# Kernel tuning notes

Hardware: AMD Instinct MI355X
Metric: run time of the kernel (lower is better)

The kernel has to match this reference:

```python
import jax, jax.numpy as jnp
from jax import lax
import numpy as np

B, T = 256, 100
N_FEAT, V, E, H = 64, 32, 8, 512
CAT_POS = np.arange(0, N_FEAT, 4)                                 # 16 categorical feature indices
CONT_POS = np.array([k for k in range(N_FEAT) if k % 4 != 0])      # 48 continuous feature indices
N_CAT, N_CONT = len(CAT_POS), len(CONT_POS)
IN_LEN = N_FEAT + N_CAT * (E - 1)                                  # 176, matches input_linear.in_features
N_LAYERS = 2                                                        # len(hidden_layers) - 1 LSTMs

# Precompute the interleaved output layout of embed(): walking feature index k,
# categorical features occupy E slots, continuous features 1 slot.
def _layout():
    cont_off, cat_off, cur = [], [], 0
    for k in range(N_FEAT):
        if k % 4 == 0:
            cat_off.append(cur); cur += E
        else:
            cont_off.append(cur); cur += 1
    return np.array(cont_off), np.array(cat_off)
CONT_OFF, CAT_OFF = _layout()
CAT_COLS = (CAT_OFF[:, None] + np.arange(E)).ravel()               # [N_CAT*E] target columns


def lstm(x, Wih, Whh, bih, bhh):
    # PyTorch LSTM, batch_first, gate order (i, f, g, o).
    xw = jnp.einsum('bti,gi->btg', x, Wih) + bih                   # [B,T,4H] input projection (one GEMM)
    def step(carry, xw_t):
        h, c = carry
        gates = xw_t + h @ Whh.T + bhh
        i, f, g, o = jnp.split(gates, 4, axis=-1)
        c = jax.nn.sigmoid(f) * c + jax.nn.sigmoid(i) * jnp.tanh(g)
        h = jax.nn.sigmoid(o) * jnp.tanh(c)
        return (h, c), h
    h0 = jnp.zeros((x.shape[0], Whh.shape[1]), x.dtype)
    (_, _), hs = lax.scan(step, (h0, h0), jnp.swapaxes(xw, 0, 1))
    return jnp.swapaxes(hs, 0, 1)                                   # [B,T,H]


def setup_inputs() -> dict:
    key = jax.random.key(0)
    ks = jax.random.split(key, 16)
    s = 0.05
    base = jax.random.normal(ks[0], (B, T, N_FEAT), jnp.float32)
    cats = jax.random.randint(ks[1], (B, T, N_CAT), 0, V)
    x = base.at[..., CAT_POS].set(cats.astype(jnp.float32))
    return {
        'x': x,
        'scaler_mean': jax.random.normal(ks[2], (N_FEAT,), jnp.float32),
        'scaler_scale': jax.random.uniform(ks[3], (N_FEAT,), jnp.float32, minval=0.5, maxval=2.0),
        'emb': jax.random.normal(ks[4], (N_CAT, V, E), jnp.float32) * s,
        'W_in': jax.random.normal(ks[5], (IN_LEN, H), jnp.float32) * s,
        'b_in': jnp.zeros((H,), jnp.float32),
        'Wih': jax.random.normal(ks[6], (N_LAYERS, 4 * H, H), jnp.float32) * s,
        'Whh': jax.random.normal(ks[7], (N_LAYERS, 4 * H, H), jnp.float32) * s,
        'bih': jnp.zeros((N_LAYERS, 4 * H), jnp.float32),
        'bhh': jnp.zeros((N_LAYERS, 4 * H), jnp.float32),
        'W_out': jax.random.normal(ks[8], (H, N_CONT), jnp.float32) * s,
        'b_out': jnp.zeros((N_CONT,), jnp.float32),
        'W_cls': jax.random.normal(ks[9], (N_CAT, H, V), jnp.float32) * s,
        'b_cls': jnp.zeros((N_CAT, V), jnp.float32),
    }


def reference(x, scaler_mean, scaler_scale, emb, W_in, b_in, Wih, Whh, bih, bhh, W_out, b_out, W_cls, b_cls):
    # ---- embed(): vectorized replacement of the triple python loop ----
    scaled = (x - scaler_mean) / scaler_scale                      # sklearn StandardScaler.transform
    cont_vals = scaled[..., CONT_POS]                              # [B,T,48]
    idx = x[..., CAT_POS].astype(jnp.int32)                        # [B,T,16] categorical codes
    embv = emb[jnp.arange(N_CAT)[None, None, :], idx]              # [B,T,16,E] gather
    new = jnp.zeros((x.shape[0], x.shape[1], IN_LEN), x.dtype)
    new = new.at[..., CONT_OFF].set(cont_vals)
    new = new.at[..., CAT_COLS].set(embv.reshape(x.shape[0], x.shape[1], N_CAT * E))
    # ---- input linear + activation ----
    h = jax.nn.relu(new @ W_in + b_in)                             # [B,T,512]
    # ---- stacked LSTMs, activation after each ----
    for l in range(N_LAYERS):
        h = jax.nn.relu(lstm(h, Wih[l], Whh[l], bih[l], bhh[l]))
    last = h[:, -1, :]                                             # [B,512]
    cont_out = last @ W_out + b_out                                # [B,48]
    cls_out = jnp.einsum('bh,nhv->bnv', last, W_cls) + b_cls       # [B,16,32] classification heads
    return (cont_out, cls_out)
```

## Files before the change

### kernel.cpp

```cpp
#include <hip/hip_runtime.h>

#define BB 256
#define TT 100
#define HH 512
#define G4 2048
#define INL 176
#define KIN 192
#define NCAT 16
#define NCONT 48
#define VV 32
#define EE 8
#define MTOT (BB*TT)
#define GRPB 32

typedef unsigned short u16;
typedef unsigned int   u32;
typedef unsigned long long u64;
typedef __attribute__((ext_vector_type(8))) short bf16x8;
typedef __attribute__((ext_vector_type(4))) float f32x4;

__device__ __forceinline__ float bf2f(u16 u){
    union { u32 i; float f; } v; v.i = ((u32)u) << 16; return v.f;
}
__device__ __forceinline__ u16 f2bf(float f){
    union { float f; u32 i; } v; v.f = f;
    u32 b = v.i;
    b += 0x7FFFu + ((b >> 16) & 1u);
    return (u16)(b >> 16);
}
__device__ __forceinline__ float fast_tanh(float x){
    float e = __expf(2.f * x);
    return 1.f - 2.f / (e + 1.f);
}

__global__ void PredictionModel_58841051955204_kernel(
    const float* __restrict__ Win, u16* __restrict__ WinT){
    int idx = blockIdx.x*256 + threadIdx.x;
    if (idx >= HH*KIN) return;
    int h = idx / KIN, i = idx % KIN;
    WinT[idx] = (i < INL) ? f2bf(Win[i*HH + h]) : (u16)0;
}

__global__ void k_cvt(const float* __restrict__ in, u16* __restrict__ out, int n){
    int i = blockIdx.x*256 + threadIdx.x;
    if (i < n) out[i] = f2bf(in[i]);
}

__global__ void k_feat(const float* __restrict__ x, const float* __restrict__ mean,
                       const float* __restrict__ scale, const float* __restrict__ emb,
                       u16* __restrict__ feat){
    int idx = blockIdx.x*256 + threadIdx.x;
    int bt = idx >> 4, g = idx & 15;
    if (bt >= MTOT) return;
    const float* xr = x + (size_t)bt*64;
    u16* fr = feat + (size_t)bt*KIN;
    int k0 = g*4;
    int ci = (int)xr[k0];
    if (ci < 0) ci = 0;
    if (ci > VV-1) ci = VV-1;
    const float* ep = emb + (size_t)(g*VV + ci)*EE;
    int c0 = g*11;
    for (int e = 0; e < 8; e++) fr[c0+e] = f2bf(ep[e]);
    for (int j = 1; j <= 3; j++){
        int k = k0 + j;
        fr[c0 + 8 + (j-1)] = f2bf((xr[k] - mean[k]) / scale[k]);
    }
    fr[INL + g] = 0;
}

__global__ __launch_bounds__(256) void k_gemm(
    const u16* __restrict__ A, int lda,
    const u16* __restrict__ W, int K,
    const float* __restrict__ bias1, const float* __restrict__ bias2,
    void* __restrict__ out, int ldo, int kc_cnt, int do_relu, int out_half)
{
    __shared__ u16 sA[64*40];
    __shared__ u16 sB[256*40];
    int tid = threadIdx.x;
    int w = tid >> 6, lane = tid & 63, q = lane >> 4, r = lane & 15;
    int m0 = blockIdx.x * 64;
    int n0 = blockIdx.y * 256;

    f32x4 acc[4][4];
    for (int a_ = 0; a_ < 4; a_++)
        for (int b_ = 0; b_ < 4; b_++){
            acc[a_][b_][0] = 0.f; acc[a_][b_][1] = 0.f;
            acc[a_][b_][2] = 0.f; acc[a_][b_][3] = 0.f;
        }

    for (int kc = 0; kc < kc_cnt; kc++){
        {
            int row = tid >> 2, seg = tid & 3;
            uint4 v = *(const uint4*)(A + (size_t)(m0+row)*lda + kc*32 + seg*8);
            *(uint4*)(&sA[row*40 + seg*8]) = v;
            const u16* wr = W + (size_t)(n0 + tid)*K + kc*32;
            uint4 b0 = *(const uint4*)(wr);
            uint4 b1 = *(const uint4*)(wr+8);
            uint4 b2 = *(const uint4*)(wr+16);
            uint4 b3 = *(const uint4*)(wr+24);
            u16* d = &sB[tid*40];
            *(uint4*)(d)    = b0; *(uint4*)(d+8)  = b1;
            *(uint4*)(d+16) = b2; *(uint4*)(d+24) = b3;
        }
        __syncthreads();
        bf16x8 a[4], b[4];
        for (int mt = 0; mt < 4; mt++) a[mt] = *(const bf16x8*)(&sA[(mt*16 + r)*40 + q*8]);
        for (int i = 0; i < 4; i++)    b[i]  = *(const bf16x8*)(&sB[((w*4+i)*16 + r)*40 + q*8]);
        for (int mt = 0; mt < 4; mt++)
            for (int i = 0; i < 4; i++)
                acc[mt][i] = __builtin_amdgcn_mfma_f32_16x16x32_bf16(a[mt], b[i], acc[mt][i], 0, 0, 0);
        __syncthreads();
    }

    for (int i = 0; i < 4; i++){
        int n = n0 + (w*4+i)*16 + r;
        float bs = 0.f;
        if (bias1) bs += bias1[n];
        if (bias2) bs += bias2[n];
        for (int mt = 0; mt < 4; mt++){
            for (int reg = 0; reg < 4; reg++){
                int m = m0 + mt*16 + q*4 + reg;
                float v = acc[mt][i][reg] + bs;
                if (do_relu) v = fmaxf(v, 0.f);
                if (out_half) ((_Float16*)out)[(size_t)m*ldo + n] = (_Float16)v;
                else          ((u16*)out)[(size_t)m*ldo + n] = f2bf(v);
            }
        }
    }
}

__global__ void k_zcnt(int* bar){
    int i = blockIdx.x*256 + threadIdx.x;
    if (i < 2*4*GRPB*16) bar[i] = 0;
}

__global__ __launch_bounds__(256, 1) void k_rec2(
    const u16* __restrict__ Whhb,
    const u16* __restrict__ Wihb1,
    const _Float16* __restrict__ xw,
    const float* __restrict__ bih, const float* __restrict__ bhh,
    u64* __restrict__ h0A, u64* __restrict__ h0B,
    u64* __restrict__ x0r,
    u64* __restrict__ h1A, u64* __restrict__ h1B,
    int* __restrict__ bar)
{
    extern __shared__ u16 smem[];
    int tid = threadIdx.x;
    int w = tid >> 6, lane = tid & 63, q = lane >> 4, r = lane & 15;
    int lay  = blockIdx.x >> 7;
    int bid7 = blockIdx.x & 127;
    int mg = bid7 & 3, jb = bid7 >> 2;
    int m0 = mg*64, j0 = jb*16;
    int j = j0 + r;
    int* F0 = bar + mg*(GRPB*16);
    int* F1 = bar + 4*(GRPB*16) + mg*(GRPB*16);

    {
        int row = tid >> 2, seg = tid & 3;
        int g = row >> 4, jj = row & 15;
        const u16* srcW = Whhb + (size_t)lay*G4*HH + (size_t)(g*HH + j0 + jj)*HH;
        u16* sW = smem + (lay ? 64*512 : 0);
        for (int i = 0; i < 16; i++){
            int c = seg*16 + i;
            *(uint4*)(&sW[row*512 + ((c ^ (row & 7)) * 8)]) = *(const uint4*)(srcW + c*8);
        }
        if (lay){
            const u16* srcI = Wihb1 + (size_t)(g*HH + j0 + jj)*HH;
            for (int i = 0; i < 16; i++){
                int c = seg*16 + i;
                *(uint4*)(&smem[row*512 + ((c ^ (row & 7)) * 8)]) = *(const uint4*)(srcI + c*8);
            }
        }
    }
    float creg[4] = {0.f, 0.f, 0.f, 0.f};
    {
        u64* hz = lay ? h1A : h0A;
        if ((r & 3) == 0){
            for (int reg = 0; reg < 4; reg++){
                int m = m0 + w*16 + q*4 + reg;
                __hip_atomic_store(&hz[(size_t)m*(HH/4) + ((j0 + r) >> 2)], 0ULL,
                                   __ATOMIC_RELAXED, __HIP_MEMORY_SCOPE_AGENT);
            }
        }
    }
    float bs1[4] = {0.f, 0.f, 0.f, 0.f};
    if (lay){
        for (int g = 0; g < 4; g++)
            bs1[g] = bih[G4 + g*HH + j] + bhh[G4 + g*HH + j];
    }
    float xnxt[4][4];
    if (!lay){
        #pragma unroll
        for (int reg = 0; reg < 4; reg++){
            int m = m0 + w*16 + q*4 + reg;
            const _Float16* xr = xw + ((size_t)m*TT + 0)*G4 + j;
            #pragma unroll
            for (int g = 0; g < 4; g++)
                xnxt[reg][g] = (float)__builtin_nontemporal_load(xr + g*HH);
        }
    }

    for (int t = -1; t < TT; t++){
        if (t >= 0 && !lay){
            const u64* hsrc = (t & 1) ? h0B : h0A;
            u64*       hdst = (t & 1) ? h0A : h0B;
            u32* xdst32 = (u32*)(x0r + (size_t)(t & 3)*BB*(HH/4));
            const u64* hrow = hsrc + (size_t)(m0 + w*16 + r)*(HH/4);

            float xcur[4][4];
            #pragma unroll
            for (int reg = 0; reg < 4; reg++)
                #pragma unroll
                for (int g = 0; g < 4; g++)
                    xcur[reg][g] = xnxt[reg][g];

            u64 hd[32];
            #pragma unroll
            for (int kc = 0; kc < 16; kc++){
                int jg0 = kc*8 + q*2;
                hd[kc*2]   = __hip_atomic_load(&hrow[jg0],   __ATOMIC_RELAXED, __HIP_MEMORY_SCOPE_AGENT);
                hd[kc*2+1] = __hip_atomic_load(&hrow[jg0+1], __ATOMIC_RELAXED, __HIP_MEMORY_SCOPE_AGENT);
            }
            if (t + 1 < TT){
                #pragma unroll
                for (int reg = 0; reg < 4; reg++){
                    int m = m0 + w*16 + q*4 + reg;
                    const _Float16* xr = xw + ((size_t)m*TT + (t+1))*G4 + j;
                    #pragma unroll
                    for (int g = 0; g < 4; g++)
                        xnxt[reg][g] = (float)__builtin_nontemporal_load(xr + g*HH);
                }
            }
            asm volatile("" :
                "+v"(hd[0]),  "+v"(hd[1]),  "+v"(hd[2]),  "+v"(hd[3]),
                "+v"(hd[4]),  "+v"(hd[5]),  "+v"(hd[6]),  "+v"(hd[7]),
                "+v"(hd[8]),  "+v"(hd[9]),  "+v"(hd[10]), "+v"(hd[11]),
                "+v"(hd[12]), "+v"(hd[13]), "+v"(hd[14]), "+v"(hd[15]));
            asm volatile("" :
                "+v"(hd[16]), "+v"(hd[17]), "+v"(hd[18]), "+v"(hd[19]),
                "+v"(hd[20]), "+v"(hd[21]), "+v"(hd[22]), "+v"(hd[23]),
                "+v"(hd[24]), "+v"(hd[25]), "+v"(hd[26]), "+v"(hd[27]),
                "+v"(hd[28]), "+v"(hd[29]), "+v"(hd[30]), "+v"(hd[31]));
            __builtin_amdgcn_sched_barrier(0);

            f32x4 acc[4];
            for (int g = 0; g < 4; g++){
                acc[g][0] = 0.f; acc[g][1] = 0.f; acc[g][2] = 0.f; acc[g][3] = 0.f;
            }
            #pragma unroll
            for (int kc = 0; kc < 16; kc++){
                union { u64 d[2]; bf16x8 v; } au;
                au.d[0] = hd[kc*2];
                au.d[1] = hd[kc*2+1];
                int cbase = kc*4 + q;
                #pragma unroll
                for (int g = 0; g < 4; g++){
                    int row = g*16 + r;
                    bf16x8 b = *(const bf16x8*)(&smem[row*512 + ((cbase ^ (row & 7)) * 8)]);
                    acc[g] = __builtin_amdgcn_mfma_f32_16x16x32_bf16(au.v, b, acc[g], 0, 0, 0);
                }
            }

            u32* hdst32 = (u32*)hdst;
            #pragma unroll
            for (int reg = 0; reg < 4; reg++){
                int m = m0 + w*16 + q*4 + reg;
                float Gi = acc[0][reg] + xcur[reg][0];
                float Gf = acc[1][reg] + xcur[reg][1];
                float Gg = acc[2][reg] + xcur[reg][2];
                float Go = acc[3][reg] + xcur[reg][3];
                float iv = 1.f/(1.f + __expf(-Gi));
                float fv = 1.f/(1.f + __expf(-Gf));
                float gv = fast_tanh(Gg);
                float ov = 1.f/(1.f + __expf(-Go));
                float c = fv * creg[reg] + iv * gv;
                creg[reg] = c;
                float h = ov * fast_tanh(c);
                u32 own  = (u32)f2bf(h);
                u32 ownr = (u32)f2bf(fmaxf(h, 0.f));
                u32 p01  = own  | (((u32)__shfl_xor((int)own,  1)) << 16);
                u32 pr01 = ownr | (((u32)__shfl_xor((int)ownr, 1)) << 16);
                if ((r & 1) == 0){
                    size_t ofs = (size_t)m*(HH/2) + ((j0 + r) >> 1);
                    __hip_atomic_store(&hdst32[ofs], p01, __ATOMIC_RELAXED, __HIP_MEMORY_SCOPE_AGENT);
                    __hip_atomic_store(&xdst32[ofs], pr01, __ATOMIC_RELAXED, __HIP_MEMORY_SCOPE_AGENT);
                }
            }
        } else if (t >= 0 && lay){
            const u64* xsrc = x0r + (size_t)(t & 3)*BB*(HH/4);
            const u64* hsrc = (t & 1) ? h1B : h1A;
            u64*       hdst = (t & 1) ? h1A : h1B;
            const u64* xrow = xsrc + (size_t)(m0 + w*16 + r)*(HH/4);
            const u64* hrow = hsrc + (size_t)(m0 + w*16 + r)*(HH/4);
            const u16* sWih = smem;
            const u16* sWhh = smem + 64*512;

            u64 hx[32], hh[32];
            #pragma unroll
            for (int kc = 0; kc < 16; kc++){
                int jg0 = kc*8 + q*2;
                hx[kc*2]   = __hip_atomic_load(&xrow[jg0],   __ATOMIC_RELAXED, __HIP_MEMORY_SCOPE_AGENT);
                hx[kc*2+1] = __hip_atomic_load(&xrow[jg0+1], __ATOMIC_RELAXED, __HIP_MEMORY_SCOPE_AGENT);
            }
            #pragma unroll
            for (int kc = 0; kc < 16; kc++){
                int jg0 = kc*8 + q*2;
                hh[kc*2]   = __hip_atomic_load(&hrow[jg0],   __ATOMIC_RELAXED, __HIP_MEMORY_SCOPE_AGENT);
                hh[kc*2+1] = __hip_atomic_load(&hrow[jg0+1], __ATOMIC_RELAXED, __HIP_MEMORY_SCOPE_AGENT);
            }
            asm volatile("" :
                "+v"(hx[0]),  "+v"(hx[1]),  "+v"(hx[2]),  "+v"(hx[3]),
                "+v"(hx[4]),  "+v"(hx[5]),  "+v"(hx[6]),  "+v"(hx[7]),
                "+v"(hx[8]),  "+v"(hx[9]),  "+v"(hx[10]), "+v"(hx[11]),
                "+v"(hx[12]), "+v"(hx[13]), "+v"(hx[14]), "+v"(hx[15]));
            asm volatile("" :
                "+v"(hx[16]), "+v"(hx[17]), "+v"(hx[18]), "+v"(hx[19]),
                "+v"(hx[20]), "+v"(hx[21]), "+v"(hx[22]), "+v"(hx[23]),
                "+v"(hx[24]), "+v"(hx[25]), "+v"(hx[26]), "+v"(hx[27]),
                "+v"(hx[28]), "+v"(hx[29]), "+v"(hx[30]), "+v"(hx[31]));
            __builtin_amdgcn_sched_barrier(0);

            f32x4 acc[4];
            for (int g = 0; g < 4; g++){
                acc[g][0] = 0.f; acc[g][1] = 0.f; acc[g][2] = 0.f; acc[g][3] = 0.f;
            }
            #pragma unroll
            for (int kc = 0; kc < 16; kc++){
                union { u64 d[2]; bf16x8 v; } au;
                au.d[0] = hx[kc*2];
                au.d[1] = hx[kc*2+1];
                int cbase = kc*4 + q;
                #pragma unroll
                for (int g = 0; g < 4; g++){
                    int row = g*16 + r;
                    bf16x8 b = *(const bf16x8*)(&sWih[row*512 + ((cbase ^ (row & 7)) * 8)]);
                    acc[g] = __builtin_amdgcn_mfma_f32_16x16x32_bf16(au.v, b, acc[g], 0, 0, 0);
                }
            }
            asm volatile("" :
                "+v"(hh[0]),  "+v"(hh[1]),  "+v"(hh[2]),  "+v"(hh[3]),
                "+v"(hh[4]),  "+v"(hh[5]),  "+v"(hh[6]),  "+v"(hh[7]),
                "+v"(hh[8]),  "+v"(hh[9]),  "+v"(hh[10]), "+v"(hh[11]),
                "+v"(hh[12]), "+v"(hh[13]), "+v"(hh[14]), "+v"(hh[15]));
            asm volatile("" :
                "+v"(hh[16]), "+v"(hh[17]), "+v"(hh[18]), "+v"(hh[19]),
                "+v"(hh[20]), "+v"(hh[21]), "+v"(hh[22]), "+v"(hh[23]),
                "+v"(hh[24]), "+v"(hh[25]), "+v"(hh[26]), "+v"(hh[27]),
                "+v"(hh[28]), "+v"(hh[29]), "+v"(hh[30]), "+v"(hh[31]));
            #pragma unroll
            for (int kc = 0; kc < 16; kc++){
                union { u64 d[2]; bf16x8 v; } au;
                au.d[0] = hh[kc*2];
                au.d[1] = hh[kc*2+1];
                int cbase = kc*4 + q;
                #pragma unroll
                for (int g = 0; g < 4; g++){
                    int row = g*16 + r;
                    bf16x8 b = *(const bf16x8*)(&sWhh[row*512 + ((cbase ^ (row & 7)) * 8)]);
                    acc[g] = __builtin_amdgcn_mfma_f32_16x16x32_bf16(au.v, b, acc[g], 0, 0, 0);
                }
            }

            u32* hdst32 = (u32*)hdst;
            #pragma unroll
            for (int reg = 0; reg < 4; reg++){
                int m = m0 + w*16 + q*4 + reg;
                float Gi = acc[0][reg] + bs1[0];
                float Gf = acc[1][reg] + bs1[1];
                float Gg = acc[2][reg] + bs1[2];
                float Go = acc[3][reg] + bs1[3];
                float iv = 1.f/(1.f + __expf(-Gi));
                float fv = 1.f/(1.f + __expf(-Gf));
                float gv = fast_tanh(Gg);
                float ov = 1.f/(1.f + __expf(-Go));
                float c = fv * creg[reg] + iv * gv;
                creg[reg] = c;
                float h = ov * fast_tanh(c);
                u32 own = (u32)f2bf(h);
                u32 p01 = own | (((u32)__shfl_xor((int)own, 1)) << 16);
                if ((r & 1) == 0){
                    __hip_atomic_store(&hdst32[(size_t)m*(HH/2) + ((j0 + r) >> 1)], p01,
                                       __ATOMIC_RELAXED, __HIP_MEMORY_SCOPE_AGENT);
                }
            }
        }

        __syncthreads();
        if (tid == 0){
            int* my = lay ? &F1[jb*16] : &F0[jb*16];
            __hip_atomic_store(my, t + 2, __ATOMIC_RELAXED, __HIP_MEMORY_SCOPE_AGENT);
        }
        if (t + 1 < TT){
            if (tid < 64){
                int* fp; int thr;
                if (!lay){
                    if (lane < GRPB){ fp = &F0[lane*16];          thr = t + 2; }
                    else            { fp = &F1[(lane-GRPB)*16];   thr = t - 1; }
                } else {
                    if (lane < GRPB){ fp = &F1[lane*16];          thr = t + 2; }
                    else            { fp = &F0[(lane-GRPB)*16];   thr = t + 3; }
                }
                long long t0c = clock64();
                while (__hip_atomic_load(fp, __ATOMIC_RELAXED, __HIP_MEMORY_SCOPE_AGENT) < thr){
                    __builtin_amdgcn_s_sleep(1);
                    if (clock64() - t0c > 50000000LL) break;
                }
            }
            __syncthreads();
        }
    }
}

__global__ void k_heads(
    const u16* __restrict__ hfin, const float* __restrict__ Wout,
    const float* __restrict__ bout, const float* __restrict__ Wcls,
    const float* __restrict__ bcls, float* __restrict__ out)
{
    __shared__ float last[HH];
    int b = blockIdx.x, tid = threadIdx.x;
    for (int h = tid; h < HH; h += 256) last[h] = fmaxf(bf2f(hfin[b*HH + h]), 0.f);
    __syncthreads();
    for (int o = tid; o < NCONT + NCAT*VV; o += 256){
        if (o < NCONT){
            float a = bout[o];
            for (int h = 0; h < HH; h++) a += last[h] * Wout[h*NCONT + o];
            out[b*NCONT + o] = (a == 0.0f) ? 7.0f : a;
        } else {
            int oc = o - NCONT;
            int n = oc >> 5, v = oc & 31;
            float a = bcls[oc];
            const float* wp = Wcls + (size_t)n*HH*VV + v;
            for (int h = 0; h < HH; h++) a += last[h] * wp[h*VV];
            out[BB*NCONT + b*(NCAT*VV) + oc] = (a == 0.0f) ? 7.0f : a;
        }
    }
}

extern "C" void kernel_launch(void* const* d_in, const int* in_sizes, int n_in,
                              void* d_out, int out_size, void* d_ws, size_t ws_size,
                              hipStream_t stream){
    const float* x      = (const float*)d_in[0];
    const float* smean  = (const float*)d_in[1];
    const float* sscale = (const float*)d_in[2];
    const float* emb    = (const float*)d_in[3];
    const float* Win    = (const float*)d_in[4];
    const float* bin    = (const float*)d_in[5];
    const float* Wih    = (const float*)d_in[6];
    const float* Whh    = (const float*)d_in[7];
    const float* bih    = (const float*)d_in[8];
    const float* bhh    = (const float*)d_in[9];
    const float* Wout   = (const float*)d_in[10];
    const float* bout   = (const float*)d_in[11];
    const float* Wcls   = (const float*)d_in[12];
    const float* bcls   = (const float*)d_in[13];
    (void)in_sizes; (void)n_in; (void)out_size;

    char* ws = (char*)d_ws;
    size_t off = 0;
    u16*      feat  = (u16*)(ws + off);      off += (size_t)MTOT*KIN*2;
    u16*      WinTb = (u16*)(ws + off);      off += (size_t)HH*KIN*2;
    u16*      Xbuf  = (u16*)(ws + off);      off += (size_t)MTOT*HH*2;
    _Float16* xw    = (_Float16*)(ws + off); off += (size_t)MTOT*G4*2;
    u16*      Wihb  = (u16*)(ws + off);      off += (size_t)2*G4*HH*2;
    u16*      Whhb  = (u16*)(ws + off);      off += (size_t)2*G4*HH*2;
    u64*      h0A   = (u64*)(ws + off);      off += (size_t)BB*HH*2;
    u64*      h0B   = (u64*)(ws + off);      off += (size_t)BB*HH*2;
    u64*      h1A   = (u64*)(ws + off);      off += (size_t)BB*HH*2;
    u64*      h1B   = (u64*)(ws + off);      off += (size_t)BB*HH*2;
    u64*      x0r   = (u64*)(ws + off);      off += (size_t)4*BB*HH*2;
    int*      bar   = (int*)(ws + off);      off += 2*4*GRPB*16*4;
    (void)off; (void)ws_size;

    PredictionModel_58841051955204_kernel<<<384, 256, 0, stream>>>(Win, WinTb);
    k_cvt<<<8192, 256, 0, stream>>>(Wih, Wihb, 2*G4*HH);
    k_cvt<<<8192, 256, 0, stream>>>(Whh, Whhb, 2*G4*HH);

    k_feat<<<1600, 256, 0, stream>>>(x, smean, sscale, emb, feat);
    k_gemm<<<dim3(400, 2), 256, 0, stream>>>(feat, KIN, WinTb, KIN, bin, (const float*)0,
                                             Xbuf, HH, 6, 1, 0);
    k_gemm<<<dim3(400, 8), 256, 0, stream>>>(Xbuf, HH, Wihb, HH, bih, bhh,
                                             xw, G4, 16, 0, 1);
    k_zcnt<<<16, 256, 0, stream>>>(bar);
    k_rec2<<<256, 256, 131072, stream>>>(Whhb, Wihb + (size_t)G4*HH, xw, bih, bhh,
                                         h0A, h0B, x0r, h1A, h1B, bar);
    k_heads<<<256, 256, 0, stream>>>((const u16*)h1A, Wout, bout, Wcls, bcls, (float*)d_out);
}
```

Before: 1.407 ms.

## Restructure wavefront LSTM recurrence: split layer loops, precompute Whh·h early

Layer 0 now writes only the raw hidden state into a 4-slot ring, and layer 1 applies ReLU on load with a bitwise bf16 mask. This removes the second ReLU'd copy that layer 0 used to write. Layer 1 computes its recurrent Whh·h product right after its own barrier, before waiting for layer 0's next output, which takes that product off the critical path between layers. Barrier flags move to per-block slots with an explicit start handshake and finer per-layer waits, which adds code complexity and some sync risk.

After: 1.535 ms. 1.09x slower.

```diff
diff --git a/kernel.cpp b/kernel.cpp
--- a/kernel.cpp
+++ b/kernel.cpp
@@ -12,6 +12,7 @@
 #define EE 8
 #define MTOT (BB*TT)
 #define GRPB 32
+#define FS 16
 
 typedef unsigned short u16;
 typedef unsigned int   u32;
@@ -31,6 +32,11 @@
 __device__ __forceinline__ float fast_tanh(float x){
     float e = __expf(2.f * x);
     return 1.f - 2.f / (e + 1.f);
+}
+__device__ __forceinline__ u64 relu4_bf16(u64 v){
+    u64 s = v & 0x8000800080008000ULL;
+    u64 m = s - (s >> 15);
+    return v & ~(s | m);
 }
 
 __global__ void PredictionModel_58841051955204_kernel(
@@ -131,7 +137,8 @@
 
 __global__ void k_zcnt(int* bar){
     int i = blockIdx.x*256 + threadIdx.x;
-    if (i < 2*4*GRPB*16) bar[i] = 0;
+    if (i < 4096)
+        __hip_atomic_store(&bar[i], 0, __ATOMIC_RELAXED, __HIP_MEMORY_SCOPE_AGENT);
 }
 
 __global__ __launch_bounds__(256, 1) void k_rec2(
@@ -139,8 +146,7 @@
     const u16* __restrict__ Wihb1,
     const _Float16* __restrict__ xw,
     const float* __restrict__ bih, const float* __restrict__ bhh,
-    u64* __restrict__ h0A, u64* __restrict__ h0B,
-    u64* __restrict__ x0r,
+    u64* __restrict__ h0r,
     u64* __restrict__ h1A, u64* __restrict__ h1B,
     int* __restrict__ bar)
 {
@@ -152,8 +158,9 @@
     int mg = bid7 & 3, jb = bid7 >> 2;
     int m0 = mg*64, j0 = jb*16;
     int j = j0 + r;
-    int* F0 = bar + mg*(GRPB*16);
-    int* F1 = bar + 4*(GRPB*16) + mg*(GRPB*16);
+    int* F0x = bar;
+    int* F1x = bar + 2048;
+    int fidx = (mg*GRPB + jb)*FS;
 
     {
         int row = tid >> 2, seg = tid & 3;
@@ -173,23 +180,31 @@
         }
     }
     float creg[4] = {0.f, 0.f, 0.f, 0.f};
-    {
-        u64* hz = lay ? h1A : h0A;
-        if ((r & 3) == 0){
-            for (int reg = 0; reg < 4; reg++){
-                int m = m0 + w*16 + q*4 + reg;
-                __hip_atomic_store(&hz[(size_t)m*(HH/4) + ((j0 + r) >> 2)], 0ULL,
-                                   __ATOMIC_RELAXED, __HIP_MEMORY_SCOPE_AGENT);
-            }
-        }
-    }
-    float bs1[4] = {0.f, 0.f, 0.f, 0.f};
-    if (lay){
-        for (int g = 0; g < 4; g++)
-            bs1[g] = bih[G4 + g*HH + j] + bhh[G4 + g*HH + j];
-    }
-    float xnxt[4][4];
+    if (!lay && (r & 3) == 0){
+        u64* hz = h0r + (size_t)3*BB*(HH/4);
+        for (int reg = 0; reg < 4; reg++){
+            int m = m0 + w*16 + q*4 + reg;
+            __hip_atomic_store(&hz[(size_t)m*(HH/4) + ((j0 + r) >> 2)], 0ULL,
+                               __ATOMIC_RELAXED, __HIP_MEMORY_SCOPE_AGENT);
+        }
+    }
+    asm volatile("s_waitcnt vmcnt(0)" ::: "memory");
+    __syncthreads();
+    if (tid == 0)
+        __hip_atomic_store(lay ? &F1x[fidx] : &F0x[fidx], 1,
+                           __ATOMIC_RELAXED, __HIP_MEMORY_SCOPE_AGENT);
+    if (tid < GRPB){
+        int* fp = (lay ? F1x : F0x) + (mg*GRPB + tid)*FS;
+        long long t0c = clock64();
+        while (__hip_atomic_load(fp, __ATOMIC_RELAXED, __HIP_MEMORY_SCOPE_AGENT) < 1){
+            __builtin_amdgcn_s_sleep(1);
+            if (clock64() - t0c > 50000000LL) break;
+        }
+    }
+    __syncthreads();
+
     if (!lay){
+        float xnxt[4][4];
         #pragma unroll
         for (int reg = 0; reg < 4; reg++){
             int m = m0 + w*16 + q*4 + reg;
@@ -198,13 +213,10 @@
             for (int g = 0; g < 4; g++)
                 xnxt[reg][g] = (float)__builtin_nontemporal_load(xr + g*HH);
         }
-    }
-
-    for (int t = -1; t < TT; t++){
-        if (t >= 0 && !lay){
-            const u64* hsrc = (t & 1) ? h0B : h0A;
-            u64*       hdst = (t & 1) ? h0A : h0B;
-            u32* xdst32 = (u32*)(x0r + (size_t)(t & 3)*BB*(HH/4));
+
+        for (int t = 0; t < TT; t++){
+            const u64* hsrc = h0r + (size_t)((t + 3) & 3)*BB*(HH/4);
+            u32* hdst32 = (u32*)(h0r + (size_t)(t & 3)*BB*(HH/4));
             const u64* hrow = hsrc + (size_t)(m0 + w*16 + r)*(HH/4);
 
             float xcur[4][4];
@@ -261,7 +273,6 @@
                 }
             }
 
-            u32* hdst32 = (u32*)hdst;
             #pragma unroll
             for (int reg = 0; reg < 4; reg++){
                 int m = m0 + w*16 + q*4 + reg;
@@ -276,37 +287,65 @@
                 float c = fv * creg[reg] + iv * gv;
                 creg[reg] = c;
                 float h = ov * fast_tanh(c);
-                u32 own  = (u32)f2bf(h);
-                u32 ownr = (u32)f2bf(fmaxf(h, 0.f));
-                u32 p01  = own  | (((u32)__shfl_xor((int)own,  1)) << 16);
-                u32 pr01 = ownr | (((u32)__shfl_xor((int)ownr, 1)) << 16);
+                u32 own = (u32)f2bf(h);
+                u32 p01 = own | (((u32)__shfl_xor((int)own, 1)) << 16);
                 if ((r & 1) == 0){
-                    size_t ofs = (size_t)m*(HH/2) + ((j0 + r) >> 1);
-                    __hip_atomic_store(&hdst32[ofs], p01, __ATOMIC_RELAXED, __HIP_MEMORY_SCOPE_AGENT);
-                    __hip_atomic_store(&xdst32[ofs], pr01, __ATOMIC_RELAXED, __HIP_MEMORY_SCOPE_AGENT);
-                }
-            }
-        } else if (t >= 0 && lay){
-            const u64* xsrc = x0r + (size_t)(t & 3)*BB*(HH/4);
-            const u64* hsrc = (t & 1) ? h1B : h1A;
+                    __hip_atomic_store(&hdst32[(size_t)m*(HH/2) + ((j0 + r) >> 1)], p01,
+                                       __ATOMIC_RELAXED, __HIP_MEMORY_SCOPE_AGENT);
+                }
+            }
+
+            asm volatile("s_waitcnt vmcnt(0)" ::: "memory");
+            __syncthreads();
+            if (tid == 0)
+                __hip_atomic_store(&F0x[fidx], t + 2, __ATOMIC_RELAXED, __HIP_MEMORY_SCOPE_AGENT);
+            if (t + 1 < TT){
+                if (tid < 64){
+                    long long t0c = clock64();
+                    const int* fp; int thr;
+                    if (lane < GRPB){ fp = &F0x[(mg*GRPB + lane)*FS];        thr = t + 2; }
+                    else            { fp = &F1x[(mg*GRPB + (lane-GRPB))*FS]; thr = t - 1; }
+                    while (__hip_atomic_load(fp, __ATOMIC_RELAXED, __HIP_MEMORY_SCOPE_AGENT) < thr){
+                        __builtin_amdgcn_s_sleep(1);
+                        if (clock64() - t0c > 50000000LL) break;
+                    }
+                }
+                __syncthreads();
+            }
+        }
+    } else {
+        const u16* sWih = smem;
+        const u16* sWhh = smem + 64*512;
+        float bs1[4];
+        for (int g = 0; g < 4; g++)
+            bs1[g] = bih[G4 + g*HH + j] + bhh[G4 + g*HH + j];
+
+        if (tid < GRPB){
+            const int* fp = &F0x[(mg*GRPB + tid)*FS];
+            long long t0c = clock64();
+            while (__hip_atomic_load(fp, __ATOMIC_RELAXED, __HIP_MEMORY_SCOPE_AGENT) < 2){
+                __builtin_amdgcn_s_sleep(1);
+                if (clock64() - t0c > 50000000LL) break;
+            }
+        }
+        __syncthreads();
+
+        f32x4 acc_hh[4];
+        for (int g = 0; g < 4; g++){
+            acc_hh[g][0] = 0.f; acc_hh[g][1] = 0.f; acc_hh[g][2] = 0.f; acc_hh[g][3] = 0.f;
+        }
+
+        for (int t = 0; t < TT; t++){
+            const u64* xsrc = h0r + (size_t)(t & 3)*BB*(HH/4);
             u64*       hdst = (t & 1) ? h1A : h1B;
             const u64* xrow = xsrc + (size_t)(m0 + w*16 + r)*(HH/4);
-            const u64* hrow = hsrc + (size_t)(m0 + w*16 + r)*(HH/4);
-            const u16* sWih = smem;
-            const u16* sWhh = smem + 64*512;
-
-            u64 hx[32], hh[32];
+
+            u64 hx[32];
             #pragma unroll
             for (int kc = 0; kc < 16; kc++){
                 int jg0 = kc*8 + q*2;
-                hx[kc*2]   = __hip_atomic_load(&xrow[jg0],   __ATOMIC_RELAXED, __HIP_MEMORY_SCOPE_AGENT);
-                hx[kc*2+1] = __hip_atomic_load(&xrow[jg0+1], __ATOMIC_RELAXED, __HIP_MEMORY_SCOPE_AGENT);
-            }
-            #pragma unroll
-            for (int kc = 0; kc < 16; kc++){
-                int jg0 = kc*8 + q*2;
-                hh[kc*2]   = __hip_atomic_load(&hrow[jg0],   __ATOMIC_RELAXED, __HIP_MEMORY_SCOPE_AGENT);
-                hh[kc*2+1] = __hip_atomic_load(&hrow[jg0+1], __ATOMIC_RELAXED, __HIP_MEMORY_SCOPE_AGENT);
+                hx[kc*2]   = relu4_bf16(__hip_atomic_load(&xrow[jg0],   __ATOMIC_RELAXED, __HIP_MEMORY_SCOPE_AGENT));
+                hx[kc*2+1] = relu4_bf16(__hip_atomic_load(&xrow[jg0+1], __ATOMIC_RELAXED, __HIP_MEMORY_SCOPE_AGENT));
             }
             asm volatile("" :
                 "+v"(hx[0]),  "+v"(hx[1]),  "+v"(hx[2]),  "+v"(hx[3]),
@@ -321,9 +360,7 @@
             __builtin_amdgcn_sched_barrier(0);
 
             f32x4 acc[4];
-            for (int g = 0; g < 4; g++){
-                acc[g][0] = 0.f; acc[g][1] = 0.f; acc[g][2] = 0.f; acc[g][3] = 0.f;
-            }
+            for (int g = 0; g < 4; g++) acc[g] = acc_hh[g];
             #pragma unroll
             for (int kc = 0; kc < 16; kc++){
                 union { u64 d[2]; bf16x8 v; } au;
@@ -334,29 +371,6 @@
                 for (int g = 0; g < 4; g++){
                     int row = g*16 + r;
                     bf16x8 b = *(const bf16x8*)(&sWih[row*512 + ((cbase ^ (row & 7)) * 8)]);
-                    acc[g] = __builtin_amdgcn_mfma_f32_16x16x32_bf16(au.v, b, acc[g], 0, 0, 0);
-                }
-            }
-            asm volatile("" :
-                "+v"(hh[0]),  "+v"(hh[1]),  "+v"(hh[2]),  "+v"(hh[3]),
-                "+v"(hh[4]),  "+v"(hh[5]),  "+v"(hh[6]),  "+v"(hh[7]),
-                "+v"(hh[8]),  "+v"(hh[9]),  "+v"(hh[10]), "+v"(hh[11]),
-                "+v"(hh[12]), "+v"(hh[13]), "+v"(hh[14]), "+v"(hh[15]));
-            asm volatile("" :
-                "+v"(hh[16]), "+v"(hh[17]), "+v"(hh[18]), "+v"(hh[19]),
-                "+v"(hh[20]), "+v"(hh[21]), "+v"(hh[22]), "+v"(hh[23]),
-                "+v"(hh[24]), "+v"(hh[25]), "+v"(hh[26]), "+v"(hh[27]),
-                "+v"(hh[28]), "+v"(hh[29]), "+v"(hh[30]), "+v"(hh[31]));
-            #pragma unroll
-            for (int kc = 0; kc < 16; kc++){
-                union { u64 d[2]; bf16x8 v; } au;
-                au.d[0] = hh[kc*2];
-                au.d[1] = hh[kc*2+1];
-                int cbase = kc*4 + q;
-                #pragma unroll
-                for (int g = 0; g < 4; g++){
-                    int row = g*16 + r;
-                    bf16x8 b = *(const bf16x8*)(&sWhh[row*512 + ((cbase ^ (row & 7)) * 8)]);
                     acc[g] = __builtin_amdgcn_mfma_f32_16x16x32_bf16(au.v, b, acc[g], 0, 0, 0);
                 }
             }
@@ -383,30 +397,71 @@
                                        __ATOMIC_RELAXED, __HIP_MEMORY_SCOPE_AGENT);
                 }
             }
-        }
-
-        __syncthreads();
-        if (tid == 0){
-            int* my = lay ? &F1[jb*16] : &F0[jb*16];
-            __hip_atomic_store(my, t + 2, __ATOMIC_RELAXED, __HIP_MEMORY_SCOPE_AGENT);
-        }
-        if (t + 1 < TT){
-            if (tid < 64){
-                int* fp; int thr;
-                if (!lay){
-                    if (lane < GRPB){ fp = &F0[lane*16];          thr = t + 2; }
-                    else            { fp = &F1[(lane-GRPB)*16];   thr = t - 1; }
-                } else {
-                    if (lane < GRPB){ fp = &F1[lane*16];          thr = t + 2; }
-                    else            { fp = &F0[(lane-GRPB)*16];   thr = t + 3; }
-                }
-                long long t0c = clock64();
-                while (__hip_atomic_load(fp, __ATOMIC_RELAXED, __HIP_MEMORY_SCOPE_AGENT) < thr){
-                    __builtin_amdgcn_s_sleep(1);
-                    if (clock64() - t0c > 50000000LL) break;
-                }
-            }
+
+            asm volatile("s_waitcnt vmcnt(0)" ::: "memory");
             __syncthreads();
+            if (tid == 0)
+                __hip_atomic_store(&F1x[fidx], t + 2, __ATOMIC_RELAXED, __HIP_MEMORY_SCOPE_AGENT);
+
+            if (t + 1 < TT){
+                if (tid < GRPB){
+                    const int* fp = &F1x[(mg*GRPB + tid)*FS];
+                    long long t0c = clock64();
+                    while (__hip_atomic_load(fp, __ATOMIC_RELAXED, __HIP_MEMORY_SCOPE_AGENT) < t + 2){
+                        __builtin_amdgcn_s_sleep(1);
+                        if (clock64() - t0c > 50000000LL) break;
+                    }
+                }
+                __syncthreads();
+
+                const u64* hrow = hdst + (size_t)(m0 + w*16 + r)*(HH/4);
+                u64 hh[32];
+                #pragma unroll
+                for (int kc = 0; kc < 16; kc++){
+                    int jg0 = kc*8 + q*2;
+                    hh[kc*2]   = __hip_atomic_load(&hrow[jg0],   __ATOMIC_RELAXED, __HIP_MEMORY_SCOPE_AGENT);
+                    hh[kc*2+1] = __hip_atomic_load(&hrow[jg0+1], __ATOMIC_RELAXED, __HIP_MEMORY_SCOPE_AGENT);
+                }
+                asm volatile("" :
+                    "+v"(hh[0]),  "+v"(hh[1]),  "+v"(hh[2]),  "+v"(hh[3]),
+                    "+v"(hh[4]),  "+v"(hh[5]),  "+v"(hh[6]),  "+v"(hh[7]),
+                    "+v"(hh[8]),  "+v"(hh[9]),  "+v"(hh[10]), "+v"(hh[11]),
+                    "+v"(hh[12]), "+v"(hh[13]), "+v"(hh[14]), "+v"(hh[15]));
+                asm volatile("" :
+                    "+v"(hh[16]), "+v"(hh[17]), "+v"(hh[18]), "+v"(hh[19]),
+                    "+v"(hh[20]), "+v"(hh[21]), "+v"(hh[22]), "+v"(hh[23]),
+                    "+v"(hh[24]), "+v"(hh[25]), "+v"(hh[26]), "+v"(hh[27]),
+                    "+v"(hh[28]), "+v"(hh[29]), "+v"(hh[30]), "+v"(hh[31]));
+                __builtin_amdgcn_sched_barrier(0);
+
+                for (int g = 0; g < 4; g++){
+                    acc_hh[g][0] = 0.f; acc_hh[g][1] = 0.f;
+                    acc_hh[g][2] = 0.f; acc_hh[g][3] = 0.f;
+                }
+                #pragma unroll
+                for (int kc = 0; kc < 16; kc++){
+                    union { u64 d[2]; bf16x8 v; } au;
+                    au.d[0] = hh[kc*2];
+                    au.d[1] = hh[kc*2+1];
+                    int cbase = kc*4 + q;
+                    #pragma unroll
+                    for (int g = 0; g < 4; g++){
+                        int row = g*16 + r;
+                        bf16x8 b = *(const bf16x8*)(&sWhh[row*512 + ((cbase ^ (row & 7)) * 8)]);
+                        acc_hh[g] = __builtin_amdgcn_mfma_f32_16x16x32_bf16(au.v, b, acc_hh[g], 0, 0, 0);
+                    }
+                }
+
+                if (tid < GRPB){
+                    const int* fp = &F0x[(mg*GRPB + tid)*FS];
+                    long long t0c = clock64();
+                    while (__hip_atomic_load(fp, __ATOMIC_RELAXED, __HIP_MEMORY_SCOPE_AGENT) < t + 3){
+                        __builtin_amdgcn_s_sleep(1);
+                        if (clock64() - t0c > 50000000LL) break;
+                    }
+                }
+                __syncthreads();
+            }
         }
     }
 }
@@ -463,12 +518,10 @@
     _Float16* xw    = (_Float16*)(ws + off); off += (size_t)MTOT*G4*2;
     u16*      Wihb  = (u16*)(ws + off);      off += (size_t)2*G4*HH*2;
     u16*      Whhb  = (u16*)(ws + off);      off += (size_t)2*G4*HH*2;
-    u64*      h0A   = (u64*)(ws + off);      off += (size_t)BB*HH*2;
-    u64*      h0B   = (u64*)(ws + off);      off += (size_t)BB*HH*2;
+    u64*      h0r   = (u64*)(ws + off);      off += (size_t)4*BB*HH*2;
     u64*      h1A   = (u64*)(ws + off);      off += (size_t)BB*HH*2;
     u64*      h1B   = (u64*)(ws + off);      off += (size_t)BB*HH*2;
-    u64*      x0r   = (u64*)(ws + off);      off += (size_t)4*BB*HH*2;
-    int*      bar   = (int*)(ws + off);      off += 2*4*GRPB*16*4;
+    int*      bar   = (int*)(ws + off);      off += 4096*4;
     (void)off; (void)ws_size;
 
     PredictionModel_58841051955204_kernel<<<384, 256, 0, stream>>>(Win, WinTb);
@@ -482,6 +535,6 @@
                                              xw, G4, 16, 0, 1);
     k_zcnt<<<16, 256, 0, stream>>>(bar);
     k_rec2<<<256, 256, 131072, stream>>>(Whhb, Wihb + (size_t)G4*HH, xw, bih, bhh,
-                                         h0A, h0B, x0r, h1A, h1B, bar);
+                                         h0r, h1A, h1B, bar);
     k_heads<<<256, 256, 0, stream>>>((const u16*)h1A, Wout, bout, Wcls, bcls, (float*)d_out);
 }
```
